# Kernel tuning notes

Hardware: AMD Instinct MI355X
Metric: run time of the kernel (lower is better)

The kernel has to match this reference:

```python
import jax, jax.numpy as jnp
import numpy as np

NG = 8       # GroupNorm groups
EPS = 1e-5   # torch default eps for GroupNorm/BatchNorm
M_AND = 5    # Anderson history size
MAX_ITER = 25
LAM = 1e-4
BETA = 1.0


def conv2d(x, w):
    # x: [B,C,H,W], w: [O,I,3,3], stride 1, SAME padding (pad=1)
    return jax.lax.conv_general_dilated(x, w, (1, 1), 'SAME',
                                        dimension_numbers=('NCHW', 'OIHW', 'NCHW'))


def group_norm(x, g, b):
    B, C, H, W = x.shape
    xg = x.reshape(B, NG, C // NG, H, W)
    mu = xg.mean((2, 3, 4), keepdims=True)
    var = xg.var((2, 3, 4), keepdims=True)
    xn = ((xg - mu) * jax.lax.rsqrt(var + EPS)).reshape(B, C, H, W)
    return xn * g[None, :, None, None] + b[None, :, None, None]


def batch_norm(x, g, b):
    # training-mode BatchNorm2d: batch statistics over (B,H,W)
    mu = x.mean((0, 2, 3), keepdims=True)
    var = x.var((0, 2, 3), keepdims=True)
    return (x - mu) * jax.lax.rsqrt(var + EPS) * g[None, :, None, None] + b[None, :, None, None]


def resnet_f(p, z, x):
    # y = norm1(relu(conv1(z))); out = norm3(relu(z + norm2(x + conv2(y))))
    y = group_norm(jax.nn.relu(conv2d(z, p['conv1_w'])), p['gn1_g'], p['gn1_b'])
    return group_norm(jax.nn.relu(z + group_norm(x + conv2d(y, p['conv2_w']),
                                                 p['gn2_g'], p['gn2_b'])),
                      p['gn3_g'], p['gn3_b'])


def anderson(f, x0, m=M_AND, lam=LAM, max_iter=MAX_ITER, beta=BETA):
    # Anderson acceleration for fixed point z = f(z); fixed iteration count
    # (the torch version early-exits at tol=0.01; we run the full max_iter for
    # a deterministic jit-friendly reference).
    shape = x0.shape
    bsz = shape[0]
    flat = lambda v: v.reshape(bsz, -1)
    X = [None] * m
    Fv = [None] * m
    X[0] = flat(x0)
    Fv[0] = flat(f(x0))
    X[1] = Fv[0]
    Fv[1] = flat(f(Fv[0].reshape(shape)))
    for k in range(2, max_iter):
        n = min(k, m)
        Xn = jnp.stack(X[:n], 1)   # [B,n,D]
        Fn = jnp.stack(Fv[:n], 1)  # [B,n,D]
        G = Fn - Xn
        Hm = jnp.einsum('bnd,bmd->bnm', G, G) + lam * jnp.eye(n, dtype=x0.dtype)
        Hb = (jnp.zeros((bsz, n + 1, n + 1), x0.dtype)
              .at[:, 1:, 1:].set(Hm)
              .at[:, 0, 1:].set(1.0)
              .at[:, 1:, 0].set(1.0))
        y = jnp.zeros((bsz, n + 1), x0.dtype).at[:, 0].set(1.0)
        alpha = jnp.linalg.solve(Hb, y[..., None])[:, 1:, 0]  # [B,n]
        xk = beta * jnp.einsum('bn,bnd->bd', alpha, Fn) + (1.0 - beta) * jnp.einsum('bn,bnd->bd', alpha, Xn)
        X[k % m] = xk
        Fv[k % m] = flat(f(xk.reshape(shape)))
    return X[(max_iter - 1) % m].reshape(shape)


def setup_inputs() -> dict:
    key = jax.random.key(0)
    ks = jax.random.split(key, 6)
    B, H, W = 8, 128, 200
    f32 = jnp.float32
    return {
        'x': jax.random.normal(ks[0], (B, 1, H, W), f32),
        'conv0_w': jax.random.normal(ks[1], (48, 1, 3, 3), f32) * 0.1,
        'conv0_b': jnp.zeros((48,), f32),
        'bn_g': jnp.ones((48,), f32),
        'bn_b': jnp.zeros((48,), f32),
        'conv1_w': jax.random.normal(ks[2], (64, 48, 3, 3), f32) * 0.01,
        'conv2_w': jax.random.normal(ks[3], (48, 64, 3, 3), f32) * 0.01,
        'gn1_g': jnp.ones((64,), f32), 'gn1_b': jnp.zeros((64,), f32),
        'gn2_g': jnp.ones((48,), f32), 'gn2_b': jnp.zeros((48,), f32),
        'gn3_g': jnp.ones((48,), f32), 'gn3_b': jnp.zeros((48,), f32),
        'fc_w': jax.random.normal(ks[4], (10, 200), f32) * 0.05,
        'fc_b': jnp.zeros((10,), f32),
    }


def reference(x, conv0_w, conv0_b, bn_g, bn_b, conv1_w, conv2_w,
              gn1_g, gn1_b, gn2_g, gn2_b, gn3_g, gn3_b, fc_w, fc_b):
    fp = {'conv1_w': conv1_w, 'conv2_w': conv2_w,
          'gn1_g': gn1_g, 'gn1_b': gn1_b,
          'gn2_g': gn2_g, 'gn2_b': gn2_b,
          'gn3_g': gn3_g, 'gn3_b': gn3_b}
    h = batch_norm(conv2d(x, conv0_w) + conv0_b[None, :, None, None], bn_g, bn_b)
    z_star = anderson(lambda z: resnet_f(fp, z, h), jnp.zeros_like(h))
    z = resnet_f(fp, z_star, h)  # one extra application, as in DEQFixedPoint
    # Linear(200,10) acts on last dim: [B,48,H,200] -> [B,48,H,10]
    return jnp.einsum('bchw,ow->bcho', z, fc_w) + fc_b
```

## Files before the change

kernel.cpp:

```cpp
#include <hip/hip_runtime.h>

#define BB   8
#define HH   128
#define WW   200
#define HWSZ 25600
#define C48  48
#define C64  64
#define NGRP 8
#define EPSV 1e-5f
#define LAMV 1e-4
#define SLOT 9830400
#define DPB  1228800
#define Y64SZ 13107200
#define BIGELEMS 131072000ull

typedef unsigned short bf16_t;
typedef __attribute__((ext_vector_type(4))) short s4v;
typedef __attribute__((ext_vector_type(8))) short s8v;
typedef __attribute__((ext_vector_type(16))) float f32x16;

__device__ inline float b2f(bf16_t b) { return __uint_as_float(((unsigned)b) << 16); }
__device__ inline bf16_t f2b(float f) {
    unsigned u = __float_as_uint(f);
    unsigned r = u + 0x7fffu + ((u >> 16) & 1u);
    return (bf16_t)(r >> 16);
}
__device__ inline float lo16(unsigned u) { return __uint_as_float(u << 16); }
__device__ inline float hi16(unsigned u) { return __uint_as_float(u & 0xffff0000u); }
__device__ inline unsigned pack2(float lo, float hi) {
    return ((unsigned)f2b(lo)) | (((unsigned)f2b(hi)) << 16);
}
__device__ inline float4 ld4(const bf16_t* p) {
    ushort4 u = *(const ushort4*)p;
    return make_float4(b2f(u.x), b2f(u.y), b2f(u.z), b2f(u.w));
}
__device__ inline void st4(bf16_t* p, float4 v) {
    ushort4 u; u.x = f2b(v.x); u.y = f2b(v.y); u.z = f2b(v.z); u.w = f2b(v.w);
    *(ushort4*)p = u;
}
__device__ inline void ld8(const bf16_t* p, float* v) {
    uint4 u = *(const uint4*)p;
    v[0] = lo16(u.x); v[1] = hi16(u.x); v[2] = lo16(u.y); v[3] = hi16(u.y);
    v[4] = lo16(u.z); v[5] = hi16(u.z); v[6] = lo16(u.w); v[7] = hi16(u.w);
}
__device__ inline void st8(bf16_t* p, const float* v) {
    uint4 u;
    u.x = pack2(v[0], v[1]); u.y = pack2(v[2], v[3]);
    u.z = pack2(v[4], v[5]); u.w = pack2(v[6], v[7]);
    *(uint4*)p = u;
}

__device__ inline void ms_from(const double* __restrict__ ds, int pair, double invcnt,
                               float& mean, float& inv) {
    double s = ds[2 * pair], q = ds[2 * pair + 1];
    double m = s * invcnt;
    double v = q * invcnt - m * m;
    mean = (float)m;
    inv = (float)(1.0 / sqrt(v + (double)EPSV));
}


__global__ void zero_kernel(float* __restrict__ p, int n) {
    int i = blockIdx.x * 256 + threadIdx.x;
    if (i < n) p[i] = 0.f;
}
__global__ void fill16_kernel(float4* __restrict__ p) {
    float4 z; z.x = z.y = z.z = z.w = 0.f;
    p[(size_t)blockIdx.x * 256 + threadIdx.x] = z;
}
__global__ void copy16_kernel(float4* __restrict__ dst, const float4* __restrict__ src) {
    size_t i = (size_t)blockIdx.x * 256 + threadIdx.x;
    dst[i] = src[i];
}

__global__ void pack_kernel(const float* __restrict__ w, bf16_t* __restrict__ apk,
                            int CIN, int CO_real, int total) {
    int idx = blockIdx.x * 256 + threadIdx.x;
    if (idx >= total) return;
    int j   = idx & 7;
    int l   = (idx >> 3) & 63;
    int mt  = (idx >> 9) & 1;
    int tap = (idx >> 10) % 9;
    int kc  = idx / 9216;
    int co = mt * 32 + (l & 31);
    int ci = kc * 16 + (l >> 5) * 8 + j;
    float v = (co < CO_real) ? w[((size_t)co * CIN + ci) * 9 + tap] : 0.f;
    apk[idx] = f2b(v);
}

__global__ __launch_bounds__(256) void conv0_kernel(
    const float* __restrict__ x, const float* __restrict__ w0,
    const float* __restrict__ b0, float* __restrict__ out)
{
    __shared__ float xs[3 * 202];
    __shared__ float wt[480];
    const int tid = threadIdx.x;
    const int bI = blockIdx.x / HH, y = blockIdx.x % HH;
    for (int i = tid; i < 606; i += 256) {
        int r = i / 202, cc = i % 202;
        int gy = y + r - 1, gx = cc - 1;
        float v = 0.f;
        if ((unsigned)gy < (unsigned)HH && (unsigned)gx < (unsigned)WW)
            v = x[(size_t)bI * HWSZ + gy * WW + gx];
        xs[r * 202 + cc] = v;
    }
    for (int i = tid; i < 480; i += 256) wt[i] = (i < 432) ? w0[i] : b0[i - 432];
    __syncthreads();
    const size_t obase = (((size_t)bI * HH + y) * WW) * 48;
    for (int ch = tid; ch < 2400; ch += 256) {
        int px = (ch * 4) / 48, c0 = (ch * 4) % 48;
        float xv[3][3];
        #pragma unroll
        for (int r = 0; r < 3; r++)
            #pragma unroll
            for (int dx = 0; dx < 3; dx++)
                xv[r][dx] = xs[r * 202 + px + dx];
        float4 o;
        #pragma unroll
        for (int j = 0; j < 4; j++) {
            int c = c0 + j;
            float acc = wt[432 + c];
            #pragma unroll
            for (int r = 0; r < 3; r++)
                #pragma unroll
                for (int dx = 0; dx < 3; dx++)
                    acc = fmaf(xv[r][dx], wt[c * 9 + r * 3 + dx], acc);
            ((float*)&o)[j] = acc;
        }
        *(float4*)(out + obase + ch * 4) = o;
    }
}

__global__ void bn_stats_kernel(const float* __restrict__ src, double* __restrict__ dst)
{
    __shared__ float ss[192], qq[192];
    const int tid = threadIdx.x;
    const int c = tid % 48, r = tid / 48;
    const int b = blockIdx.y;
    const size_t base = ((size_t)b * HWSZ + (size_t)blockIdx.x * 256) * 48 + c;
    float s = 0.f, q = 0.f;
    for (int p = r; p < 256; p += 4) {
        float v = src[base + (size_t)p * 48];
        s += v; q += v * v;
    }
    ss[tid] = s; qq[tid] = q;
    __syncthreads();
    if (tid < 48) {
        s = ss[tid] + ss[tid + 48] + ss[tid + 96] + ss[tid + 144];
        q = qq[tid] + qq[tid + 48] + qq[tid + 96] + qq[tid + 144];
        unsafeAtomicAdd(&dst[tid * 2],     (double)s);
        unsafeAtomicAdd(&dst[tid * 2 + 1], (double)q);
    }
}

__global__ __launch_bounds__(256) void bn_apply_kernel(
    const float* __restrict__ src, bf16_t* __restrict__ dst,
    const float* __restrict__ gamma, const float* __restrict__ beta,
    const double* __restrict__ ds)
{
    __shared__ float gaT[48], beT[48];
    int tid = threadIdx.x;
    if (tid < 48) {
        float mean, inv; ms_from(ds, tid, 1.0 / 204800.0, mean, inv);
        float ga = gamma[tid] * inv;
        gaT[tid] = ga; beT[tid] = beta[tid] - mean * ga;
    }
    __syncthreads();
    size_t base = (size_t)blockIdx.x * 1024 + (size_t)tid * 4;
    int c0 = (int)(base % 48);
    float4 v = *(const float4*)(src + base);
    ushort4 o;
    o.x = f2b(fmaf(v.x, gaT[c0],     beT[c0]));
    o.y = f2b(fmaf(v.y, gaT[c0 + 1], beT[c0 + 1]));
    o.z = f2b(fmaf(v.z, gaT[c0 + 2], beT[c0 + 2]));
    o.w = f2b(fmaf(v.w, gaT[c0 + 3], beT[c0 + 3]));
    *(ushort4*)(dst + base) = o;
}

template<int CIN, int CIPAD, int CO, int OTS, int CG, bool RELU, bool ADDH, bool FOLDGN>
__global__ __launch_bounds__(512) void conv_mfma_kernel(
    const bf16_t* __restrict__ in, const s8v* __restrict__ apk,
    const bf16_t* __restrict__ hadd, bf16_t* __restrict__ out,
    double* __restrict__ dsOut,
    const double* __restrict__ dsPrev, const float* __restrict__ gPrev,
    const float* __restrict__ bPrev)
{
    constexpr int KC  = CIN / 16;
    constexpr int NCH = CIN / 4;
    const int tid  = threadIdx.x;
    const int lane = tid & 63;
    const int wv   = tid >> 6;
    const int x0 = blockIdx.x * 32;
    const int y0 = blockIdx.y * 8;
    const int b  = blockIdx.z;

    __shared__ __align__(16) bf16_t bt[10 * 34 * CIPAD];
    __shared__ __align__(16) float gaT[FOLDGN ? CIN : 4];
    __shared__ __align__(16) float beT[FOLDGN ? CIN : 4];
    __shared__ float ss[512], qq[512];

    if (FOLDGN) {
        if (tid < CIN) {
            float mean, inv;
            ms_from(dsPrev, b * NGRP + tid / (CIN / NGRP), 1.0 / 204800.0, mean, inv);
            float ga = gPrev[tid] * inv;
            gaT[tid] = ga; beT[tid] = bPrev[tid] - mean * ga;
        }
        __syncthreads();
    }
    for (int i = tid; i < 10 * 34 * NCH; i += 512) {
        int ch = i % NCH, p = i / NCH;
        int r = p / 34, c = p - r * 34;
        int gy = y0 + r - 1, gx = x0 + c - 1;
        ushort4 v = make_ushort4(0, 0, 0, 0);
        if ((unsigned)gy < (unsigned)HH && (unsigned)gx < (unsigned)WW) {
            ushort4 raw = *(const ushort4*)(in + ((((size_t)b * HH + gy) * WW + gx) * CIN + ch * 4));
            if (FOLDGN) {
                float4 ga4 = *(const float4*)&gaT[ch * 4];
                float4 be4 = *(const float4*)&beT[ch * 4];
                v.x = f2b(fmaf(b2f(raw.x), ga4.x, be4.x));
                v.y = f2b(fmaf(b2f(raw.y), ga4.y, be4.y));
                v.z = f2b(fmaf(b2f(raw.z), ga4.z, be4.z));
                v.w = f2b(fmaf(b2f(raw.w), ga4.w, be4.w));
            } else v = raw;
        }
        *(ushort4*)(bt + p * CIPAD + ch * 4) = v;
    }
    __syncthreads();

    const int n = lane & 31, half = lane >> 5;
    f32x16 acc0, acc1;
    #pragma unroll
    for (int i = 0; i < 16; i++) { acc0[i] = 0.f; acc1[i] = 0.f; }

    #pragma unroll
    for (int ky = 0; ky < 3; ky++)
    #pragma unroll
    for (int kx = 0; kx < 3; kx++) {
        const int tap = ky * 3 + kx;
        s8v af[2 * KC];
        #pragma unroll
        for (int kc = 0; kc < KC; kc++) {
            af[2 * kc]     = apk[(size_t)kc * 1152 + tap * 128 + lane];
            af[2 * kc + 1] = apk[(size_t)kc * 1152 + tap * 128 + 64 + lane];
        }
        const bf16_t* brow = bt + ((wv + ky) * 34 + n + kx) * CIPAD + half * 8;
        #pragma unroll
        for (int kc = 0; kc < KC; kc++) {
            s8v bfrag = *(const s8v*)(brow + kc * 16);
            acc0 = __builtin_amdgcn_mfma_f32_32x32x16_bf16(af[2 * kc],     bfrag, acc0, 0, 0, 0);
            acc1 = __builtin_amdgcn_mfma_f32_32x32x16_bf16(af[2 * kc + 1], bfrag, acc1, 0, 0, 0);
        }
    }
    __syncthreads();

    bf16_t* ot = bt;
    {
        const int pxl = wv * 32 + n;
        const bool pv = (x0 + n) < WW;
        #pragma unroll
        for (int g4 = 0; g4 < 4; g4++) {
            s4v pk0;
            #pragma unroll
            for (int jj = 0; jj < 4; jj++) {
                float v = acc0[g4 * 4 + jj];
                if (RELU) v = fmaxf(v, 0.f);
                pk0[jj] = (short)(pv ? f2b(v) : (bf16_t)0);
            }
            *(s4v*)&ot[pxl * OTS + g4 * 8 + 4 * half] = pk0;
            const int c1b = 32 + g4 * 8 + 4 * half;
            if (c1b + 3 < CO) {
                s4v pk1;
                #pragma unroll
                for (int jj = 0; jj < 4; jj++) {
                    float v = acc1[g4 * 4 + jj];
                    if (RELU) v = fmaxf(v, 0.f);
                    pk1[jj] = (short)(pv ? f2b(v) : (bf16_t)0);
                }
                *(s4v*)&ot[pxl * OTS + c1b] = pk1;
            }
        }
    }
    __syncthreads();
    {
        constexpr int NCH8 = 256 * CO / 8;
        for (int ch = tid; ch < NCH8; ch += 512) {
            int pxl = ch / (CO / 8);
            int co0 = (ch % (CO / 8)) * 8;
            int row = pxl >> 5, col = pxl & 31;
            int xx = x0 + col;
            if (xx < WW) {
                bf16_t* lp = &ot[pxl * OTS + co0];
                size_t ga = (((size_t)b * HH + y0 + row) * WW + xx) * CO + co0;
                if (ADDH) {
                    float4 h0 = ld4(hadd + ga), h1 = ld4(hadd + ga + 4);
                    float4 l0 = ld4(lp), l1 = ld4(lp + 4);
                    float4 v0 = make_float4(l0.x + h0.x, l0.y + h0.y, l0.z + h0.z, l0.w + h0.w);
                    float4 v1 = make_float4(l1.x + h1.x, l1.y + h1.y, l1.z + h1.z, l1.w + h1.w);
                    st4(out + ga, v0); st4(out + ga + 4, v1);
                    st4(lp, v0); st4(lp + 4, v1);
                } else {
                    *(ushort4*)(out + ga)     = *(ushort4*)lp;
                    *(ushort4*)(out + ga + 4) = *(ushort4*)(lp + 4);
                }
            }
        }
    }
    if (ADDH) __syncthreads();
    {
        constexpr int NPH = 512 / CO;
        const int c = tid % CO, rr = tid / CO;
        float s = 0.f, q = 0.f;
        if (rr < NPH) {
            for (int px = rr; px < 256; px += NPH) {
                float v = b2f(ot[px * OTS + c]);
                s += v; q += v * v;
            }
        }
        ss[tid] = s; qq[tid] = q;
        __syncthreads();
        if (tid < CO) {
            float S = ss[tid], Q = qq[tid];
            #pragma unroll
            for (int p = 1; p < NPH; p++) { S += ss[tid + p * CO]; Q += qq[tid + p * CO]; }
            ss[tid] = S; qq[tid] = Q;
        }
        __syncthreads();
        if (tid < NGRP) {
            float S = 0.f, Q = 0.f;
            #pragma unroll
            for (int j = 0; j < CG; j++) { S += ss[tid * CG + j]; Q += qq[tid * CG + j]; }
            unsafeAtomicAdd(&dsOut[((size_t)b * NGRP + tid) * 2],     (double)S);
            unsafeAtomicAdd(&dsOut[((size_t)b * NGRP + tid) * 2 + 1], (double)Q);
        }
    }
}

__global__ __launch_bounds__(192) void add_relu_gn2_kernel(
    bf16_t* __restrict__ u, const bf16_t* __restrict__ z,
    const double* __restrict__ ds2, const float* __restrict__ g2,
    const float* __restrict__ b2, double* __restrict__ ds3)
{
    __shared__ float sm[16];
    const int tid = threadIdx.x;
    const int c0 = 8 * (tid % 6), pxr = tid / 6;
    const int b = blockIdx.y;
    if (tid < 16) sm[tid] = 0.f;
    const int gA = c0 / 6;
    const int split = (gA + 1) * 6 - c0;
    float meanA, invA, meanB, invB;
    ms_from(ds2, b * NGRP + gA,     1.0 / 153600.0, meanA, invA);
    ms_from(ds2, b * NGRP + gA + 1, 1.0 / 153600.0, meanB, invB);
    float wga[8], wbe[8];
    #pragma unroll
    for (int e = 0; e < 8; e++) {
        int c = c0 + e;
        float m = (e < split) ? meanA : meanB, iv = (e < split) ? invA : invB;
        float ga = g2[c] * iv;
        wga[e] = ga; wbe[e] = b2[c] - m * ga;
    }
    __syncthreads();
    const size_t pxbase = (size_t)b * HWSZ + (size_t)blockIdx.x * 256;
    float sA = 0.f, qA = 0.f, sB = 0.f, qB = 0.f;
    for (int it = 0; it < 8; it++) {
        size_t idx = (pxbase + it * 32 + pxr) * 48 + c0;
        float uu[8], zz[8], vv[8];
        ld8(u + idx, uu); ld8(z + idx, zz);
        #pragma unroll
        for (int e = 0; e < 8; e++) {
            float v = fmaxf(fmaf(uu[e], wga[e], wbe[e]) + zz[e], 0.f);
            vv[e] = v;
            if (e < split) { sA += v; qA += v * v; } else { sB += v; qB += v * v; }
        }
        st8(u + idx, vv);
    }
    atomicAdd(&sm[2 * gA], sA);     atomicAdd(&sm[2 * gA + 1], qA);
    atomicAdd(&sm[2 * gA + 2], sB); atomicAdd(&sm[2 * gA + 3], qB);
    __syncthreads();
    if (tid < NGRP) {
        unsafeAtomicAdd(&ds3[(b * NGRP + tid) * 2],     (double)sm[tid * 2]);
        unsafeAtomicAdd(&ds3[(b * NGRP + tid) * 2 + 1], (double)sm[tid * 2 + 1]);
    }
}

__global__ __launch_bounds__(192) void gn3_gram_kernel(
    const bf16_t* __restrict__ v, const bf16_t* __restrict__ z,
    bf16_t* __restrict__ F, bf16_t* __restrict__ G,
    const double* __restrict__ ds3, const float* __restrict__ g3,
    const float* __restrict__ b3,
    const bf16_t* __restrict__ Gall, int jslot, int nf, double* __restrict__ gram)
{
    __shared__ double red[3][5];
    const int tid = threadIdx.x;
    const int c0 = 8 * (tid % 6), pxr = tid / 6;
    const int b = blockIdx.y;
    const int gA = c0 / 6;
    const int split = (gA + 1) * 6 - c0;
    float meanA, invA, meanB, invB;
    ms_from(ds3, b * NGRP + gA,     1.0 / 153600.0, meanA, invA);
    ms_from(ds3, b * NGRP + gA + 1, 1.0 / 153600.0, meanB, invB);
    float wga[8], wbe[8];
    #pragma unroll
    for (int e = 0; e < 8; e++) {
        int c = c0 + e;
        float m = (e < split) ? meanA : meanB, iv = (e < split) ? invA : invB;
        float ga = g3[c] * iv;
        wga[e] = ga; wbe[e] = b3[c] - m * ga;
    }
    const size_t pxbase = (size_t)b * HWSZ + (size_t)blockIdx.x * 256;
    double dot[5] = {0.0, 0.0, 0.0, 0.0, 0.0};
    for (int it = 0; it < 8; it++) {
        size_t idx = (pxbase + it * 32 + pxr) * 48 + c0;
        float rr[8];
        ld8(v + idx, rr);
        #pragma unroll
        for (int e = 0; e < 8; e++) rr[e] = fmaf(rr[e], wga[e], wbe[e]);
        st8(F + idx, rr);
        if (nf > 0) {
            float zz[8], gg[8];
            ld8(z + idx, zz);
            #pragma unroll
            for (int e = 0; e < 8; e++) gg[e] = rr[e] - zz[e];
            st8(G + idx, gg);
            #pragma unroll
            for (int i = 0; i < 5; i++) {
                if (i >= nf) continue;
                float d = 0.f;
                if (i == jslot) {
                    #pragma unroll
                    for (int e = 0; e < 8; e++) d = fmaf(gg[e], gg[e], d);
                } else {
                    float gi[8];
                    ld8(Gall + (size_t)i * SLOT + idx, gi);
                    #pragma unroll
                    for (int e = 0; e < 8; e++) d = fmaf(gg[e], gi[e], d);
                }
                dot[i] += (double)d;
            }
        }
    }
    if (nf > 0) {
        #pragma unroll
        for (int i = 0; i < 5; i++) {
            if (i >= nf) continue;
            #pragma unroll
            for (int off = 32; off > 0; off >>= 1) dot[i] += __shfl_down(dot[i], off);
        }
        int wv = tid >> 6;
        if ((tid & 63) == 0) {
            #pragma unroll
            for (int i = 0; i < 5; i++) if (i < nf) red[wv][i] = dot[i];
        }
        __syncthreads();
        if (tid == 0) {
            #pragma unroll
            for (int i = 0; i < 5; i++) {
                if (i >= nf) continue;
                double D = red[0][i] + red[1][i] + red[2][i];
                unsafeAtomicAdd(&gram[b * 25 + jslot * 5 + i], D);
                if (i != jslot) unsafeAtomicAdd(&gram[b * 25 + i * 5 + jslot], D);
            }
        }
    }
}


__global__ void solve_kernel(const double* __restrict__ gram, float* __restrict__ alpha, int n) {
    int b = threadIdx.x;
    if (b >= BB) return;
    const int m = n + 1;
    double A[6][7];
    for (int i = 0; i < m; i++)
        for (int jj = 0; jj <= m; jj++) A[i][jj] = 0.0;
    for (int i = 1; i < m; i++) { A[0][i] = 1.0; A[i][0] = 1.0; }
    for (int i = 1; i < m; i++)
        for (int jj = 1; jj < m; jj++)
            A[i][jj] = gram[b * 25 + (i - 1) * 5 + (jj - 1)] + ((i == jj) ? LAMV : 0.0);
    A[0][m] = 1.0;
    for (int col = 0; col < m; col++) {
        int piv = col; double best = fabs(A[col][col]);
        for (int rr = col + 1; rr < m; rr++) {
            double tv = fabs(A[rr][col]);
            if (tv > best) { best = tv; piv = rr; }
        }
        if (piv != col)
            for (int cc = col; cc <= m; cc++) {
                double tmp = A[col][cc]; A[col][cc] = A[piv][cc]; A[piv][cc] = tmp;
            }
        double invp = 1.0 / A[col][col];
        for (int cc = col; cc <= m; cc++) A[col][cc] *= invp;
        for (int rr = 0; rr < m; rr++) {
            if (rr == col) continue;
            double f = A[rr][col];
            if (f != 0.0)
                for (int cc = col; cc <= m; cc++) A[rr][cc] = fma(-f, A[col][cc], A[rr][cc]);
        }
    }
    for (int i = 0; i < n; i++) alpha[b * 5 + i] = (float)A[i + 1][m];
}

__global__ __launch_bounds__(256) void xk_kernel(
    const bf16_t* __restrict__ Fb, const float* __restrict__ alpha,
    bf16_t* __restrict__ zcur, int n, double* __restrict__ gram, int jz, int nf)
{
    if (blockIdx.x == 0 && threadIdx.x < 8 * nf) {
        int b = threadIdx.x / nf, i = threadIdx.x % nf;
        gram[b * 25 + jz * 5 + i] = 0.0;
        gram[b * 25 + i * 5 + jz] = 0.0;
    }
    const int b = blockIdx.x / 75;
    float al[5];
    #pragma unroll
    for (int j = 0; j < 5; j++) al[j] = (j < n) ? alpha[b * 5 + j] : 0.f;
    const size_t base = (size_t)blockIdx.x * 16384 + (size_t)threadIdx.x * 8;
    for (int it = 0; it < 8; it++) {
        size_t idx = base + (size_t)it * 2048;
        float s[8] = {0.f, 0.f, 0.f, 0.f, 0.f, 0.f, 0.f, 0.f};
        #pragma unroll
        for (int j = 0; j < 5; j++) {
            if (j < n) {
                float f[8];
                ld8(Fb + (size_t)j * SLOT + idx, f);
                #pragma unroll
                for (int e = 0; e < 8; e++) s[e] = fmaf(f[e], al[j], s[e]);
            }
        }
        st8(zcur + idx, s);
    }
}

__global__ __launch_bounds__(512) void fc_kernel(
    const bf16_t* __restrict__ zf, const float* __restrict__ fw,
    const float* __restrict__ fb, float* __restrict__ out)
{
    __shared__ bf16_t row[9600];
    __shared__ float fwT[2000];
    int tid = threadIdx.x;
    int b = blockIdx.x >> 7, hh = blockIdx.x & 127;
    size_t base = (((size_t)b * HH + hh) * WW) * 48;
    for (int i = tid; i < 2400; i += 512)
        *(ushort4*)&row[i * 4] = *(const ushort4*)(zf + base + (size_t)i * 4);
    for (int i = tid; i < 2000; i += 512) fwT[i] = fw[i];
    __syncthreads();
    if (tid < 480) {
        int c = tid % 48, o = tid / 48;
        float acc = fb[o];
        #pragma unroll 4
        for (int w = 0; w < 200; w++)
            acc = fmaf(b2f(row[w * 48 + c]), fwT[o * 200 + w], acc);
        out[(((size_t)b * 48 + c) * HH + hh) * 10 + o] = acc;
    }
}


static inline int imin(int a, int b) { return a < b ? a : b; }

extern "C" void kernel_launch(void* const* d_in, const int* in_sizes, int n_in,
                              void* d_out, int out_size, void* d_ws, size_t ws_size,
                              hipStream_t stream)
{
    const float* x   = (const float*)d_in[0];
    const float* w0  = (const float*)d_in[1];
    const float* b0  = (const float*)d_in[2];
    const float* bng = (const float*)d_in[3];
    const float* bnb = (const float*)d_in[4];
    const float* w1  = (const float*)d_in[5];
    const float* w2  = (const float*)d_in[6];
    const float* g1  = (const float*)d_in[7];
    const float* be1 = (const float*)d_in[8];
    const float* g2  = (const float*)d_in[9];
    const float* be2 = (const float*)d_in[10];
    const float* g3  = (const float*)d_in[11];
    const float* be3 = (const float*)d_in[12];
    const float* fcw = (const float*)d_in[13];
    const float* fcb = (const float*)d_in[14];
    float* out = (float*)d_out;

    bf16_t* h    = (bf16_t*)d_ws;
    bf16_t* zcur = h + (size_t)SLOT;
    bf16_t* y64  = zcur + (size_t)SLOT;
    bf16_t* Fb   = y64 + (size_t)Y64SZ;
    bf16_t* Gb   = Fb + 5 * (size_t)SLOT;
    double* dstats = (double*)((char*)d_ws + BIGELEMS * 2);
    double* gram   = dstats + 9696;
    float*  alpha  = (float*)(gram + 200);
    bf16_t* apk1   = (bf16_t*)(alpha + 40);
    bf16_t* apk2   = apk1 + 27648;
    float*  scratch = (float*)Gb;

    const size_t need = BIGELEMS * 2 + 9696 * 8 + 200 * 8 + 40 * 4 + (27648 + 36864) * 2;
    if (ws_size < need) return;

    const dim3 blk(256);
    const int CHUNKS16 = SLOT * 2 / 16 / 256;

    zero_kernel<<<(19792 + 255) / 256, blk, 0, stream>>>((float*)dstats, 19792);
    pack_kernel<<<108, blk, 0, stream>>>(w1, apk1, 48, 64, 27648);
    pack_kernel<<<144, blk, 0, stream>>>(w2, apk2, 64, 48, 36864);
    fill16_kernel<<<CHUNKS16, blk, 0, stream>>>((float4*)zcur);

    conv0_kernel<<<BB * HH, blk, 0, stream>>>(x, w0, b0, scratch);
    bn_stats_kernel<<<dim3(100, BB), dim3(192), 0, stream>>>(scratch, dstats);
    bn_apply_kernel<<<SLOT / 1024, blk, 0, stream>>>(scratch, h, bng, bnb, dstats);

    int call = 0;
    auto resnet = [&](const bf16_t* zin, bf16_t* Fdst, bf16_t* Gdst, int jslot, int nf) {
        double* ds = dstats + 96 + 384 * call;
        call++;
        dim3 cg(7, 16, BB);
        conv_mfma_kernel<48, 56, 64, 66, 8, true, false, false><<<cg, dim3(512), 0, stream>>>(
            zin, (const s8v*)apk1, nullptr, y64, ds, nullptr, nullptr, nullptr);
        conv_mfma_kernel<64, 72, 48, 50, 6, false, true, true><<<cg, dim3(512), 0, stream>>>(
            y64, (const s8v*)apk2, h, Fdst, ds + 128, ds, g1, be1);
        add_relu_gn2_kernel<<<dim3(100, BB), dim3(192), 0, stream>>>(
            Fdst, zin, ds + 128, g2, be2, ds + 256);
        gn3_gram_kernel<<<dim3(100, BB), dim3(192), 0, stream>>>(
            Fdst, zin, Fdst, Gdst, ds + 256, g3, be3, Gb, jslot, nf, gram);
    };

    resnet(zcur, Fb, Gb, 0, 1);
    copy16_kernel<<<CHUNKS16, blk, 0, stream>>>((float4*)zcur, (const float4*)Fb);
    resnet(zcur, Fb + (size_t)SLOT, Gb + (size_t)SLOT, 1, 2);

    for (int k = 2; k <= 24; k++) {
        int n = imin(k, 5);
        int j = k % 5;
        int nf = imin(k + 1, 5);
        solve_kernel<<<1, 64, 0, stream>>>(gram, alpha, n);
        xk_kernel<<<600, blk, 0, stream>>>(Fb, alpha, zcur, n, gram, j, nf);
        if (k < 24)
            resnet(zcur, Fb + (size_t)j * SLOT, Gb + (size_t)j * SLOT, j, nf);
    }

    resnet(zcur, Fb, nullptr, 0, 0);

    fc_kernel<<<BB * HH, dim3(512), 0, stream>>>(Fb, fcw, fcb, out);
}
```

Baseline: 4.970 ms.

## Load conv operands directly from global memory instead of staging halo tile in LDS

The conv kernel no longer stages a padded 10x34 input halo tile in shared memory. Each lane now loads its 8-channel B fragment straight from global memory for every tap, applies the GroupNorm fold in registers with packed bf16 conversion, and zeroes out-of-bounds taps. Launch bounds now request 4 blocks per SM to raise occupancy, since shared memory use drops to the output tile. The xk kernel also gets four times more blocks with less work each. The trade-off is redundant global/L2 reads, since each input pixel is fetched up to nine times, and the GN fold is recomputed per tap.

```diff
diff --git a/kernel.cpp b/kernel.cpp
--- a/kernel.cpp
+++ b/kernel.cpp
@@ -177,16 +177,15 @@
     *(ushort4*)(dst + base) = o;
 }
 
-template<int CIN, int CIPAD, int CO, int OTS, int CG, bool RELU, bool ADDH, bool FOLDGN>
-__global__ __launch_bounds__(512) void conv_mfma_kernel(
+template<int CIN, int CO, int OTS, int CG, bool RELU, bool ADDH, bool FOLDGN>
+__global__ __launch_bounds__(512, 4) void conv_direct_kernel(
     const bf16_t* __restrict__ in, const s8v* __restrict__ apk,
     const bf16_t* __restrict__ hadd, bf16_t* __restrict__ out,
     double* __restrict__ dsOut,
     const double* __restrict__ dsPrev, const float* __restrict__ gPrev,
     const float* __restrict__ bPrev)
 {
-    constexpr int KC  = CIN / 16;
-    constexpr int NCH = CIN / 4;
+    constexpr int KC = CIN / 16;
     const int tid  = threadIdx.x;
     const int lane = tid & 63;
     const int wv   = tid >> 6;
@@ -194,7 +193,7 @@
     const int y0 = blockIdx.y * 8;
     const int b  = blockIdx.z;
 
-    __shared__ __align__(16) bf16_t bt[10 * 34 * CIPAD];
+    __shared__ __align__(16) bf16_t ot[256 * OTS];
     __shared__ __align__(16) float gaT[FOLDGN ? CIN : 4];
     __shared__ __align__(16) float beT[FOLDGN ? CIN : 4];
     __shared__ float ss[512], qq[512];
@@ -208,53 +207,72 @@
         }
         __syncthreads();
     }
-    for (int i = tid; i < 10 * 34 * NCH; i += 512) {
-        int ch = i % NCH, p = i / NCH;
-        int r = p / 34, c = p - r * 34;
-        int gy = y0 + r - 1, gx = x0 + c - 1;
-        ushort4 v = make_ushort4(0, 0, 0, 0);
-        if ((unsigned)gy < (unsigned)HH && (unsigned)gx < (unsigned)WW) {
-            ushort4 raw = *(const ushort4*)(in + ((((size_t)b * HH + gy) * WW + gx) * CIN + ch * 4));
-            if (FOLDGN) {
-                float4 ga4 = *(const float4*)&gaT[ch * 4];
-                float4 be4 = *(const float4*)&beT[ch * 4];
-                v.x = f2b(fmaf(b2f(raw.x), ga4.x, be4.x));
-                v.y = f2b(fmaf(b2f(raw.y), ga4.y, be4.y));
-                v.z = f2b(fmaf(b2f(raw.z), ga4.z, be4.z));
-                v.w = f2b(fmaf(b2f(raw.w), ga4.w, be4.w));
-            } else v = raw;
-        }
-        *(ushort4*)(bt + p * CIPAD + ch * 4) = v;
-    }
-    __syncthreads();
 
     const int n = lane & 31, half = lane >> 5;
+    bool vx[3]; unsigned xoff[3];
+    #pragma unroll
+    for (int kx = 0; kx < 3; kx++) {
+        int xx = x0 + n + kx - 1;
+        vx[kx] = (unsigned)xx < (unsigned)WW;
+        xoff[kx] = (unsigned)((vx[kx] ? xx : 0) * CIN);
+    }
+    bool vy[3]; unsigned rowoff[3];
+    #pragma unroll
+    for (int ky = 0; ky < 3; ky++) {
+        int gy = y0 + wv + ky - 1;
+        vy[ky] = (unsigned)gy < (unsigned)HH;
+        rowoff[ky] = (unsigned)(((b * HH + (vy[ky] ? gy : 0)) * WW) * CIN);
+    }
+    const int choff = half * 8;
+
     f32x16 acc0, acc1;
     #pragma unroll
     for (int i = 0; i < 16; i++) { acc0[i] = 0.f; acc1[i] = 0.f; }
 
-    #pragma unroll
-    for (int ky = 0; ky < 3; ky++)
-    #pragma unroll
-    for (int kx = 0; kx < 3; kx++) {
-        const int tap = ky * 3 + kx;
-        s8v af[2 * KC];
-        #pragma unroll
-        for (int kc = 0; kc < KC; kc++) {
-            af[2 * kc]     = apk[(size_t)kc * 1152 + tap * 128 + lane];
-            af[2 * kc + 1] = apk[(size_t)kc * 1152 + tap * 128 + 64 + lane];
-        }
-        const bf16_t* brow = bt + ((wv + ky) * 34 + n + kx) * CIPAD + half * 8;
-        #pragma unroll
-        for (int kc = 0; kc < KC; kc++) {
-            s8v bfrag = *(const s8v*)(brow + kc * 16);
-            acc0 = __builtin_amdgcn_mfma_f32_32x32x16_bf16(af[2 * kc],     bfrag, acc0, 0, 0, 0);
-            acc1 = __builtin_amdgcn_mfma_f32_32x32x16_bf16(af[2 * kc + 1], bfrag, acc1, 0, 0, 0);
-        }
-    }
-    __syncthreads();
-
-    bf16_t* ot = bt;
+    s8v vz;
+    #pragma unroll
+    for (int e = 0; e < 8; e++) vz[e] = 0;
+
+    #pragma unroll
+    for (int kc = 0; kc < KC; kc++) {
+        const int ch0 = kc * 16 + choff;
+        float ga8[8], be8[8];
+        if (FOLDGN) {
+            #pragma unroll
+            for (int e = 0; e < 8; e++) { ga8[e] = gaT[ch0 + e]; be8[e] = beT[ch0 + e]; }
+        }
+        #pragma unroll
+        for (int ky = 0; ky < 3; ky++) {
+            if (!vy[ky]) continue;
+            #pragma unroll
+            for (int kx = 0; kx < 3; kx++) {
+                const int tap = ky * 3 + kx;
+                s8v a0 = apk[(size_t)kc * 1152 + tap * 128 + lane];
+                s8v a1 = apk[(size_t)kc * 1152 + tap * 128 + 64 + lane];
+                s8v braw = *(const s8v*)(in + rowoff[ky] + xoff[kx] + ch0);
+                s8v bf;
+                if (FOLDGN) {
+                    float f[8];
+                    #pragma unroll
+                    for (int e = 0; e < 8; e++)
+                        f[e] = fmaf(b2f((bf16_t)(unsigned short)braw[e]), ga8[e], be8[e]);
+                    unsigned p01, p23, p45, p67;
+                    asm("v_cvt_pk_bf16_f32 %0, %1, %2" : "=v"(p01) : "v"(f[0]), "v"(f[1]));
+                    asm("v_cvt_pk_bf16_f32 %0, %1, %2" : "=v"(p23) : "v"(f[2]), "v"(f[3]));
+                    asm("v_cvt_pk_bf16_f32 %0, %1, %2" : "=v"(p45) : "v"(f[4]), "v"(f[5]));
+                    asm("v_cvt_pk_bf16_f32 %0, %1, %2" : "=v"(p67) : "v"(f[6]), "v"(f[7]));
+                    if (!vx[kx]) { p01 = 0; p23 = 0; p45 = 0; p67 = 0; }
+                    unsigned* bp = (unsigned*)&bf;
+                    bp[0] = p01; bp[1] = p23; bp[2] = p45; bp[3] = p67;
+                } else {
+                    bf = vx[kx] ? braw : vz;
+                }
+                acc0 = __builtin_amdgcn_mfma_f32_32x32x16_bf16(a0, bf, acc0, 0, 0, 0);
+                acc1 = __builtin_amdgcn_mfma_f32_32x32x16_bf16(a1, bf, acc1, 0, 0, 0);
+            }
+        }
+    }
+
     {
         const int pxl = wv * 32 + n;
         const bool pv = (x0 + n) < WW;
@@ -464,7 +482,6 @@
     }
 }
 
-
 __global__ void solve_kernel(const double* __restrict__ gram, float* __restrict__ alpha, int n) {
     int b = threadIdx.x;
     if (b >= BB) return;
@@ -508,12 +525,12 @@
         gram[b * 25 + jz * 5 + i] = 0.0;
         gram[b * 25 + i * 5 + jz] = 0.0;
     }
-    const int b = blockIdx.x / 75;
+    const int b = blockIdx.x / 300;
     float al[5];
     #pragma unroll
     for (int j = 0; j < 5; j++) al[j] = (j < n) ? alpha[b * 5 + j] : 0.f;
-    const size_t base = (size_t)blockIdx.x * 16384 + (size_t)threadIdx.x * 8;
-    for (int it = 0; it < 8; it++) {
+    const size_t base = (size_t)blockIdx.x * 4096 + (size_t)threadIdx.x * 8;
+    for (int it = 0; it < 2; it++) {
         size_t idx = base + (size_t)it * 2048;
         float s[8] = {0.f, 0.f, 0.f, 0.f, 0.f, 0.f, 0.f, 0.f};
         #pragma unroll
@@ -608,9 +625,9 @@
         double* ds = dstats + 96 + 384 * call;
         call++;
         dim3 cg(7, 16, BB);
-        conv_mfma_kernel<48, 56, 64, 66, 8, true, false, false><<<cg, dim3(512), 0, stream>>>(
+        conv_direct_kernel<48, 64, 66, 8, true, false, false><<<cg, dim3(512), 0, stream>>>(
             zin, (const s8v*)apk1, nullptr, y64, ds, nullptr, nullptr, nullptr);
-        conv_mfma_kernel<64, 72, 48, 50, 6, false, true, true><<<cg, dim3(512), 0, stream>>>(
+        conv_direct_kernel<64, 48, 50, 6, false, true, true><<<cg, dim3(512), 0, stream>>>(
             y64, (const s8v*)apk2, h, Fdst, ds + 128, ds, g1, be1);
         add_relu_gn2_kernel<<<dim3(100, BB), dim3(192), 0, stream>>>(
             Fdst, zin, ds + 128, g2, be2, ds + 256);
@@ -627,7 +644,7 @@
         int j = k % 5;
         int nf = imin(k + 1, 5);
         solve_kernel<<<1, 64, 0, stream>>>(gram, alpha, n);
-        xk_kernel<<<600, blk, 0, stream>>>(Fb, alpha, zcur, n, gram, j, nf);
+        xk_kernel<<<2400, blk, 0, stream>>>(Fb, alpha, zcur, n, gram, j, nf);
         if (k < 24)
             resnet(zcur, Fb + (size_t)j * SLOT, Gb + (size_t)j * SLOT, j, nf);
     }
```

Measured after the change: 5.240 ms. 1.05x slower.
